# Kernel optimization log

Measured on AMD Instinct MI355X. Metric: run time of the kernel, lower is better.

Reference implementation:

```python
import jax, jax.numpy as jnp
import numpy as np

B, N, D, E, R, K = 4, 2048, 1024, 8, 256, 2


def setup_inputs() -> dict:
    key = jax.random.key(0)
    ks = jax.random.split(key, 5)
    scale = 0.02
    return {
        "x": jax.random.normal(ks[0], (B, N, D), dtype=jnp.float32),
        "gate_w": jax.random.normal(ks[1], (D, E), dtype=jnp.float32) * scale,
        "Wu": jax.random.normal(ks[2], (E, D, R), dtype=jnp.float32) * scale,
        "Wv": jax.random.normal(ks[3], (E, D, R), dtype=jnp.float32) * scale,
        "Wo": jax.random.normal(ks[4], (E, R, D), dtype=jnp.float32) * scale,
    }


def reference(x, gate_w, Wu, Wv, Wo):
    # Router: top-k over expert logits, softmax over the selected k logits.
    logits = jnp.einsum("bnd,de->bne", x, gate_w)          # [B,N,E]
    topv, topi = jax.lax.top_k(logits, K)                    # [B,N,K]
    w = jax.nn.softmax(topv, axis=-1)                        # [B,N,K]

    # Dense all-expert SwiGLU (matches reference semantics: every expert
    # computed for every token, then gathered by top-k index).
    u = jnp.einsum("bnd,edr->bner", x, Wu)                  # [B,N,E,R]
    v = jnp.einsum("bnd,edr->bner", x, Wv)                  # [B,N,E,R]
    s = jax.nn.silu(u) * v                                   # [B,N,E,R]
    Y = jnp.einsum("bner,erd->bned", s, Wo)                 # [B,N,E,D]

    # Gather the k selected experts per token and combine with gate weights.
    y_sel = jnp.take_along_axis(Y, topi[..., None], axis=2)  # [B,N,K,D]
    out = jnp.einsum("bnkd,bnk->bnd", y_sel, w)             # [B,N,D]
    return out
```

## Files before the change

kernel.cpp:

```cpp
#include <hip/hip_runtime.h>
#include <math.h>

#define BN 8192
#define DIM 1024
#define NE 8
#define RR 256

using bf16x8 = __attribute__((ext_vector_type(8))) short;
using f32x4  = __attribute__((ext_vector_type(4))) float;

__device__ inline unsigned short f2bf(float f) {
    unsigned int u = __float_as_uint(f);
    u = (u + 0x7fffu + ((u >> 16) & 1u)) >> 16;
    return (unsigned short)u;
}

__global__ __launch_bounds__(256) void k_gwt(const float* __restrict__ gw,
                                             float* __restrict__ gwT) {
    int i = blockIdx.x * 256 + threadIdx.x;
    float v = gw[i];
    int d = i >> 3, e = i & 7;
    gwT[e * DIM + d] = v;
}

__global__ __launch_bounds__(256) void k_router3(const float* __restrict__ x,
                                                 const float* __restrict__ gwT,
                                                 int* __restrict__ topi,
                                                 float* __restrict__ topw,
                                                 unsigned short* __restrict__ xb) {
    int wid  = (blockIdx.x * blockDim.x + threadIdx.x) >> 6;
    int lane = threadIdx.x & 63;
    const float* xp = x + (size_t)wid * DIM + lane * 4;
    unsigned short* xbp = xb + (size_t)wid * DIM + lane * 4;
    float4 acc[NE];
#pragma unroll
    for (int e = 0; e < NE; ++e) acc[e] = float4{0.f, 0.f, 0.f, 0.f};
#pragma unroll
    for (int k = 0; k < 4; ++k) {
        float4 xv = *(const float4*)(xp + k * 256);
        ushort4 us = { f2bf(xv.x), f2bf(xv.y), f2bf(xv.z), f2bf(xv.w) };
        *(ushort4*)(xbp + k * 256) = us;
#pragma unroll
        for (int e = 0; e < NE; ++e) {
            float4 gv = *(const float4*)(gwT + e * DIM + k * 256 + lane * 4);
            acc[e].x += xv.x * gv.x; acc[e].y += xv.y * gv.y;
            acc[e].z += xv.z * gv.z; acc[e].w += xv.w * gv.w;
        }
    }
    float lg[NE];
#pragma unroll
    for (int e = 0; e < NE; ++e)
        lg[e] = (acc[e].x + acc[e].y) + (acc[e].z + acc[e].w);
#pragma unroll
    for (int off = 32; off; off >>= 1) {
#pragma unroll
        for (int e = 0; e < NE; ++e) lg[e] += __shfl_xor(lg[e], off, 64);
    }
    if (lane == 0) {
        float best = lg[0]; int bi = 0;
#pragma unroll
        for (int e = 1; e < NE; ++e) if (lg[e] > best) { best = lg[e]; bi = e; }
        float sec = -3.4e38f; int si = 0;
#pragma unroll
        for (int e = 0; e < NE; ++e) if (e != bi && lg[e] > sec) { sec = lg[e]; si = e; }
        float p  = __expf(sec - best);
        float w0 = 1.f / (1.f + p);
        float w1 = p * w0;
        topi[wid * 2 + 0] = bi;  topw[wid * 2 + 0] = w0;
        topi[wid * 2 + 1] = si;  topw[wid * 2 + 1] = w1;
    }
}

__global__ __launch_bounds__(1024) void k_count_scan(const int* __restrict__ topi,
                                                     int* __restrict__ counts,
                                                     int* __restrict__ offsets,
                                                     int* __restrict__ fill,
                                                     int* __restrict__ tileOff) {
    __shared__ int sh[1024 * NE];
    int tid = threadIdx.x;
    int c[NE];
#pragma unroll
    for (int j = 0; j < NE; ++j) c[j] = 0;
    const int4* tp = (const int4*)topi;
    for (int i = tid; i < BN * 2 / 4; i += 1024) {
        int4 v = tp[i];
#pragma unroll
        for (int j = 0; j < NE; ++j)
            c[j] += (v.x == j) + (v.y == j) + (v.z == j) + (v.w == j);
    }
#pragma unroll
    for (int j = 0; j < NE; ++j) sh[tid * NE + j] = c[j];
    __syncthreads();
    for (int s = 512; s > 0; s >>= 1) {
        if (tid < s) {
#pragma unroll
            for (int j = 0; j < NE; ++j) sh[tid * NE + j] += sh[(tid + s) * NE + j];
        }
        __syncthreads();
    }
    if (tid == 0) {
        int acc = 0, tacc = 0;
        for (int j = 0; j < NE; ++j) {
            int cj = sh[j];
            counts[j]  = cj;
            offsets[j] = acc;   acc  += cj;
            tileOff[j] = tacc;  tacc += (cj + 63) >> 6;
        }
        tileOff[NE] = tacc;
    }
    if (tid < NE) fill[tid] = 0;
}

__global__ __launch_bounds__(256) void k_fill2(const int* __restrict__ topi,
                                               const float* __restrict__ topw,
                                               const int* __restrict__ offsets,
                                               int* __restrict__ fill,
                                               int* __restrict__ btok,
                                               float* __restrict__ bw) {
    int tid = threadIdx.x;
    int i = blockIdx.x * 256 + tid;
    int w = tid >> 6, lane = tid & 63;
    int e = topi[i];
    float wt = topw[i];

    __shared__ int waveCnt[4][NE];
    __shared__ int wavePre[4][NE];
    __shared__ int baseSh[NE];

    int myrank = 0;
    unsigned long long lt = (1ull << lane) - 1ull;
#pragma unroll
    for (int j = 0; j < NE; ++j) {
        unsigned long long m = __ballot(e == j);
        if (e == j) myrank = __popcll(m & lt);
        if (lane == 0) waveCnt[w][j] = __popcll(m);
    }
    __syncthreads();
    if (tid < NE) {
        int j = tid, acc = 0;
#pragma unroll
        for (int ww = 0; ww < 4; ++ww) { wavePre[ww][j] = acc; acc += waveCnt[ww][j]; }
        baseSh[j] = atomicAdd(&fill[j], acc);
    }
    __syncthreads();
    int slot = offsets[e] + baseSh[e] + wavePre[w][e] + myrank;
    btok[slot] = i >> 1;
    bw[slot]   = wt;
}

__global__ __launch_bounds__(256) void k_cvt3(const float* __restrict__ Wu,
                                              const float* __restrict__ Wv,
                                              const float* __restrict__ Wo,
                                              unsigned short* __restrict__ Wub,
                                              unsigned short* __restrict__ Wvb,
                                              unsigned short* __restrict__ Wob) {
    int z = blockIdx.y;
    int which = z >> 3, e = z & 7;
    int tile = blockIdx.x;
    const float* in; unsigned short* out;
    int M, N, n0, m0;
    if (which < 2) {
        M = DIM; N = RR;
        n0 = (tile & 7) * 32;  m0 = (tile >> 3) * 32;
        in = which ? Wv : Wu;  out = which ? Wvb : Wub;
    } else {
        M = RR; N = DIM;
        n0 = (tile & 31) * 32; m0 = (tile >> 5) * 32;
        in = Wo; out = Wob;
    }
    __shared__ float t[32][33];
    int tx = threadIdx.x & 31, ty = threadIdx.x >> 5;
    const float* inE = in + (size_t)e * M * N;
    unsigned short* outE = out + (size_t)e * M * N;
#pragma unroll
    for (int i = ty; i < 32; i += 8)
        t[i][tx] = inE[(size_t)(m0 + i) * N + n0 + tx];
    __syncthreads();
#pragma unroll
    for (int i = ty; i < 32; i += 8)
        outE[(size_t)(n0 + i) * M + m0 + tx] = f2bf(t[tx][i]);
}

__global__ __launch_bounds__(256, 2) void k_uv(
        const unsigned short* __restrict__ xb,
        const unsigned short* __restrict__ Wub,
        const unsigned short* __restrict__ Wvb,
        const int* __restrict__ counts,
        const int* __restrict__ offsets,
        const int* __restrict__ tileOff,
        const int* __restrict__ btok,
        const float* __restrict__ bw,
        unsigned short* __restrict__ Sbuf) {
    int rt = blockIdx.x & 3;
    int mt_lin = blockIdx.x >> 2;
    if (mt_lin >= tileOff[NE]) return;
    int e = 0;
#pragma unroll
    for (int j = 1; j < NE; ++j) if (mt_lin >= tileOff[j]) e = j;
    int t0 = (mt_lin - tileOff[e]) * 64;
    int ne = counts[e];
    int nt = min(64, ne - t0);
    int start = offsets[e] + t0;

    int tid = threadIdx.x;
    int w = tid >> 6, lane = tid & 63;
    int m16 = lane & 15, quad = lane >> 4;
    int wm = w & 1, wn = w >> 1;

    __shared__ unsigned short As[64][72];
    __shared__ unsigned short Bs[128][72];
    __shared__ int   tokL[64];
    __shared__ float gwL[64];

    if (tid < 64) {
        tokL[tid] = (tid < nt) ? btok[start + tid] : btok[start];
        gwL[tid]  = (tid < nt) ? bw[start + tid] : 0.f;
    }
    __syncthreads();

    const unsigned short* WuE = Wub + (size_t)e * RR * DIM + (size_t)rt * 64 * DIM;
    const unsigned short* WvE = Wvb + (size_t)e * RR * DIM + (size_t)rt * 64 * DIM;

    int arow = tid >> 2, apart = tid & 3;
    const unsigned short* asrc = xb + (size_t)tokL[arow] * DIM + apart * 16;
    int brow = tid >> 1, bhalf = tid & 1;
    const unsigned short* bsrc =
        (brow < 64 ? WuE + (size_t)brow * DIM : WvE + (size_t)(brow - 64) * DIM)
        + bhalf * 32;

    f32x4 accU[2][2], accV[2][2];
    f32x4 zz = {0.f, 0.f, 0.f, 0.f};
#pragma unroll
    for (int mt = 0; mt < 2; ++mt)
#pragma unroll
        for (int nl = 0; nl < 2; ++nl) { accU[mt][nl] = zz; accV[mt][nl] = zz; }

    for (int k0 = 0; k0 < DIM; k0 += 64) {
        __syncthreads();
        *(uint4*)&As[arow][apart * 16]     = *(const uint4*)(asrc + k0);
        *(uint4*)&As[arow][apart * 16 + 8] = *(const uint4*)(asrc + k0 + 8);
        *(uint4*)&Bs[brow][bhalf * 32]      = *(const uint4*)(bsrc + k0);
        *(uint4*)&Bs[brow][bhalf * 32 + 8]  = *(const uint4*)(bsrc + k0 + 8);
        *(uint4*)&Bs[brow][bhalf * 32 + 16] = *(const uint4*)(bsrc + k0 + 16);
        *(uint4*)&Bs[brow][bhalf * 32 + 24] = *(const uint4*)(bsrc + k0 + 24);
        __syncthreads();
#pragma unroll
        for (int ks = 0; ks < 2; ++ks) {
            bf16x8 a[2], bu[2], bv[2];
#pragma unroll
            for (int mt = 0; mt < 2; ++mt)
                a[mt] = *(const bf16x8*)&As[wm * 32 + mt * 16 + m16][ks * 32 + quad * 8];
#pragma unroll
            for (int nl = 0; nl < 2; ++nl) {
                bu[nl] = *(const bf16x8*)&Bs[wn * 32 + nl * 16 + m16][ks * 32 + quad * 8];
                bv[nl] = *(const bf16x8*)&Bs[64 + wn * 32 + nl * 16 + m16][ks * 32 + quad * 8];
            }
#pragma unroll
            for (int nl = 0; nl < 2; ++nl)
#pragma unroll
                for (int mt = 0; mt < 2; ++mt) {
                    accU[mt][nl] = __builtin_amdgcn_mfma_f32_16x16x32_bf16(a[mt], bu[nl], accU[mt][nl], 0, 0, 0);
                    accV[mt][nl] = __builtin_amdgcn_mfma_f32_16x16x32_bf16(a[mt], bv[nl], accV[mt][nl], 0, 0, 0);
                }
        }
    }

#pragma unroll
    for (int mt = 0; mt < 2; ++mt)
#pragma unroll
        for (int nl = 0; nl < 2; ++nl)
#pragma unroll
            for (int reg = 0; reg < 4; ++reg) {
                int trow = wm * 32 + mt * 16 + quad * 4 + reg;
                int rcol = rt * 64 + wn * 32 + nl * 16 + m16;
                float u = accU[mt][nl][reg], v = accV[mt][nl][reg];
                float s = (u / (1.f + __expf(-u))) * v * gwL[trow];
                if (trow < nt)
                    Sbuf[(size_t)(start + trow) * RR + rcol] = f2bf(s);
            }
}

__global__ __launch_bounds__(256, 2) void k_down(
        const unsigned short* __restrict__ Sbuf,
        const unsigned short* __restrict__ Wob,
        const int* __restrict__ counts,
        const int* __restrict__ offsets,
        const int* __restrict__ tileOff,
        const int* __restrict__ btok,
        float* __restrict__ out) {
    int nd = blockIdx.x & 7;
    int mt_lin = blockIdx.x >> 3;
    if (mt_lin >= tileOff[NE]) return;
    int e = 0;
#pragma unroll
    for (int j = 1; j < NE; ++j) if (mt_lin >= tileOff[j]) e = j;
    int t0 = (mt_lin - tileOff[e]) * 64;
    int ne = counts[e];
    int nt = min(64, ne - t0);
    int start = offsets[e] + t0;

    int tid = threadIdx.x;
    int w = tid >> 6, lane = tid & 63;
    int m16 = lane & 15, quad = lane >> 4;
    int wm = w & 1, wn = w >> 1;

    __shared__ unsigned short As[64][72];
    __shared__ unsigned short Bs[128][72];
    __shared__ int tokL[64];

    if (tid < 64)
        tokL[tid] = (tid < nt) ? btok[start + tid] : btok[start];
    __syncthreads();

    const unsigned short* WoE = Wob + (size_t)e * DIM * RR + (size_t)nd * 128 * RR;

    int arow = tid >> 2, apart = tid & 3;
    const unsigned short* asrc = Sbuf + (size_t)(start + arow) * RR + apart * 16;
    int brow = tid >> 1, bhalf = tid & 1;
    const unsigned short* bsrc = WoE + (size_t)brow * RR + bhalf * 32;

    f32x4 acc[2][4];
    f32x4 zz = {0.f, 0.f, 0.f, 0.f};
#pragma unroll
    for (int mt = 0; mt < 2; ++mt)
#pragma unroll
        for (int nl = 0; nl < 4; ++nl) acc[mt][nl] = zz;

    for (int k0 = 0; k0 < RR; k0 += 64) {
        __syncthreads();
        *(uint4*)&As[arow][apart * 16]     = *(const uint4*)(asrc + k0);
        *(uint4*)&As[arow][apart * 16 + 8] = *(const uint4*)(asrc + k0 + 8);
        *(uint4*)&Bs[brow][bhalf * 32]      = *(const uint4*)(bsrc + k0);
        *(uint4*)&Bs[brow][bhalf * 32 + 8]  = *(const uint4*)(bsrc + k0 + 8);
        *(uint4*)&Bs[brow][bhalf * 32 + 16] = *(const uint4*)(bsrc + k0 + 16);
        *(uint4*)&Bs[brow][bhalf * 32 + 24] = *(const uint4*)(bsrc + k0 + 24);
        __syncthreads();
#pragma unroll
        for (int ks = 0; ks < 2; ++ks) {
            bf16x8 a[2], b[4];
#pragma unroll
            for (int mt = 0; mt < 2; ++mt)
                a[mt] = *(const bf16x8*)&As[wm * 32 + mt * 16 + m16][ks * 32 + quad * 8];
#pragma unroll
            for (int nl = 0; nl < 4; ++nl)
                b[nl] = *(const bf16x8*)&Bs[wn * 64 + nl * 16 + m16][ks * 32 + quad * 8];
#pragma unroll
            for (int nl = 0; nl < 4; ++nl)
#pragma unroll
                for (int mt = 0; mt < 2; ++mt)
                    acc[mt][nl] = __builtin_amdgcn_mfma_f32_16x16x32_bf16(a[mt], b[nl], acc[mt][nl], 0, 0, 0);
        }
    }

#pragma unroll
    for (int mt = 0; mt < 2; ++mt)
#pragma unroll
        for (int nl = 0; nl < 4; ++nl)
#pragma unroll
            for (int reg = 0; reg < 4; ++reg) {
                int srow = wm * 32 + mt * 16 + quad * 4 + reg;
                int d    = nd * 128 + wn * 64 + nl * 16 + m16;
                if (srow < nt)
                    atomicAdd(&out[(size_t)tokL[srow] * DIM + d], acc[mt][nl][reg]);
            }
}

extern "C" void kernel_launch(void* const* d_in, const int* in_sizes, int n_in,
                              void* d_out, int out_size, void* d_ws, size_t ws_size,
                              hipStream_t stream) {
    const float* x  = (const float*)d_in[0];
    const float* gw = (const float*)d_in[1];
    const float* Wu = (const float*)d_in[2];
    const float* Wv = (const float*)d_in[3];
    const float* Wo = (const float*)d_in[4];
    float* out = (float*)d_out;

    int*   wsi     = (int*)d_ws;
    int*   counts  = wsi + 0;
    int*   offsets = wsi + 8;
    int*   fill    = wsi + 16;
    int*   tileOff = wsi + 24;
    int*   topi    = wsi + 48;
    float* topw    = (float*)(wsi + 48 + 16384);
    int*   btok    = wsi + 48 + 32768;
    float* bw      = (float*)(wsi + 48 + 49152);
    float* gwT     = (float*)((char*)d_ws + 327808 - 64 * 1024 + 65536);
    gwT            = (float*)((char*)d_ws + 294912);

    const size_t off_xb  = 393216;
    const size_t off_wub = off_xb  + (size_t)BN * DIM * 2;
    const size_t off_wvb = off_wub + (size_t)NE * RR * DIM * 2;
    const size_t off_wob = off_wvb + (size_t)NE * RR * DIM * 2;
    const size_t off_sb  = off_wob + (size_t)NE * DIM * RR * 2;

    unsigned short* xb   = (unsigned short*)((char*)d_ws + off_xb);
    unsigned short* Wub  = (unsigned short*)((char*)d_ws + off_wub);
    unsigned short* Wvb  = (unsigned short*)((char*)d_ws + off_wvb);
    unsigned short* Wob  = (unsigned short*)((char*)d_ws + off_wob);
    unsigned short* Sbuf = (unsigned short*)((char*)d_ws + off_sb);

    hipMemsetAsync(d_out, 0, (size_t)BN * DIM * sizeof(float), stream);

    k_gwt<<<dim3(DIM * NE / 256), 256, 0, stream>>>(gw, gwT);
    k_router3<<<dim3(BN / 4), 256, 0, stream>>>(x, gwT, topi, topw, xb);
    k_count_scan<<<1, 1024, 0, stream>>>(topi, counts, offsets, fill, tileOff);
    k_fill2<<<dim3(BN * 2 / 256), 256, 0, stream>>>(topi, topw, offsets, fill, btok, bw);
    k_cvt3<<<dim3(256, 24), 256, 0, stream>>>(Wu, Wv, Wo, Wub, Wvb, Wob);

    k_uv<<<dim3(264 * 4), 256, 0, stream>>>(xb, Wub, Wvb, counts, offsets, tileOff,
                                            btok, bw, Sbuf);
    k_down<<<dim3(264 * 8), 256, 0, stream>>>(Sbuf, Wob, counts, offsets, tileOff,
                                              btok, out);
}
```

Before: 230.4 us.

## Register-prefetch next K tile in GEMMs and replace atomic scatter with combine pass

Both grouped GEMM kernels now load the next K tile from global memory into registers while the current tile is consumed from LDS, overlapping global latency with MFMA work. The down-projection also writes per-slot results into a dense float buffer instead of atomically adding into the output. A new combine kernel then sums each token's two expert rows, which also removes the output memset. This trades atomic traffic for an extra 64 MB write and read and extra register pressure. It falls back to the atomic path when the workspace is too small.

```diff
diff --git a/kernel.cpp b/kernel.cpp
--- a/kernel.cpp
+++ b/kernel.cpp
@@ -116,7 +116,8 @@
                                                const int* __restrict__ offsets,
                                                int* __restrict__ fill,
                                                int* __restrict__ btok,
-                                               float* __restrict__ bw) {
+                                               float* __restrict__ bw,
+                                               int* __restrict__ slotOf) {
     int tid = threadIdx.x;
     int i = blockIdx.x * 256 + tid;
     int w = tid >> 6, lane = tid & 63;
@@ -146,6 +147,7 @@
     int slot = offsets[e] + baseSh[e] + wavePre[w][e] + myrank;
     btok[slot] = i >> 1;
     bw[slot]   = wt;
+    slotOf[i]  = slot;
 }
 
 __global__ __launch_bounds__(256) void k_cvt3(const float* __restrict__ Wu,
@@ -235,15 +237,31 @@
 #pragma unroll
         for (int nl = 0; nl < 2; ++nl) { accU[mt][nl] = zz; accV[mt][nl] = zz; }
 
-    for (int k0 = 0; k0 < DIM; k0 += 64) {
+    uint4 pa0 = *(const uint4*)(asrc);
+    uint4 pa1 = *(const uint4*)(asrc + 8);
+    uint4 pb0 = *(const uint4*)(bsrc);
+    uint4 pb1 = *(const uint4*)(bsrc + 8);
+    uint4 pb2 = *(const uint4*)(bsrc + 16);
+    uint4 pb3 = *(const uint4*)(bsrc + 24);
+
+    for (int kt = 0; kt < 16; ++kt) {
         __syncthreads();
-        *(uint4*)&As[arow][apart * 16]     = *(const uint4*)(asrc + k0);
-        *(uint4*)&As[arow][apart * 16 + 8] = *(const uint4*)(asrc + k0 + 8);
-        *(uint4*)&Bs[brow][bhalf * 32]      = *(const uint4*)(bsrc + k0);
-        *(uint4*)&Bs[brow][bhalf * 32 + 8]  = *(const uint4*)(bsrc + k0 + 8);
-        *(uint4*)&Bs[brow][bhalf * 32 + 16] = *(const uint4*)(bsrc + k0 + 16);
-        *(uint4*)&Bs[brow][bhalf * 32 + 24] = *(const uint4*)(bsrc + k0 + 24);
+        *(uint4*)&As[arow][apart * 16]      = pa0;
+        *(uint4*)&As[arow][apart * 16 + 8]  = pa1;
+        *(uint4*)&Bs[brow][bhalf * 32]      = pb0;
+        *(uint4*)&Bs[brow][bhalf * 32 + 8]  = pb1;
+        *(uint4*)&Bs[brow][bhalf * 32 + 16] = pb2;
+        *(uint4*)&Bs[brow][bhalf * 32 + 24] = pb3;
         __syncthreads();
+        if (kt < 15) {
+            int k1 = (kt + 1) * 64;
+            pa0 = *(const uint4*)(asrc + k1);
+            pa1 = *(const uint4*)(asrc + k1 + 8);
+            pb0 = *(const uint4*)(bsrc + k1);
+            pb1 = *(const uint4*)(bsrc + k1 + 8);
+            pb2 = *(const uint4*)(bsrc + k1 + 16);
+            pb3 = *(const uint4*)(bsrc + k1 + 24);
+        }
 #pragma unroll
         for (int ks = 0; ks < 2; ++ks) {
             bf16x8 a[2], bu[2], bv[2];
@@ -287,6 +305,7 @@
         const int* __restrict__ offsets,
         const int* __restrict__ tileOff,
         const int* __restrict__ btok,
+        float* __restrict__ ybuf,
         float* __restrict__ out) {
     int nd = blockIdx.x & 7;
     int mt_lin = blockIdx.x >> 3;
@@ -326,15 +345,31 @@
 #pragma unroll
         for (int nl = 0; nl < 4; ++nl) acc[mt][nl] = zz;
 
-    for (int k0 = 0; k0 < RR; k0 += 64) {
+    uint4 pa0 = *(const uint4*)(asrc);
+    uint4 pa1 = *(const uint4*)(asrc + 8);
+    uint4 pb0 = *(const uint4*)(bsrc);
+    uint4 pb1 = *(const uint4*)(bsrc + 8);
+    uint4 pb2 = *(const uint4*)(bsrc + 16);
+    uint4 pb3 = *(const uint4*)(bsrc + 24);
+
+    for (int kt = 0; kt < 4; ++kt) {
         __syncthreads();
-        *(uint4*)&As[arow][apart * 16]     = *(const uint4*)(asrc + k0);
-        *(uint4*)&As[arow][apart * 16 + 8] = *(const uint4*)(asrc + k0 + 8);
-        *(uint4*)&Bs[brow][bhalf * 32]      = *(const uint4*)(bsrc + k0);
-        *(uint4*)&Bs[brow][bhalf * 32 + 8]  = *(const uint4*)(bsrc + k0 + 8);
-        *(uint4*)&Bs[brow][bhalf * 32 + 16] = *(const uint4*)(bsrc + k0 + 16);
-        *(uint4*)&Bs[brow][bhalf * 32 + 24] = *(const uint4*)(bsrc + k0 + 24);
+        *(uint4*)&As[arow][apart * 16]      = pa0;
+        *(uint4*)&As[arow][apart * 16 + 8]  = pa1;
+        *(uint4*)&Bs[brow][bhalf * 32]      = pb0;
+        *(uint4*)&Bs[brow][bhalf * 32 + 8]  = pb1;
+        *(uint4*)&Bs[brow][bhalf * 32 + 16] = pb2;
+        *(uint4*)&Bs[brow][bhalf * 32 + 24] = pb3;
         __syncthreads();
+        if (kt < 3) {
+            int k1 = (kt + 1) * 64;
+            pa0 = *(const uint4*)(asrc + k1);
+            pa1 = *(const uint4*)(asrc + k1 + 8);
+            pb0 = *(const uint4*)(bsrc + k1);
+            pb1 = *(const uint4*)(bsrc + k1 + 8);
+            pb2 = *(const uint4*)(bsrc + k1 + 16);
+            pb3 = *(const uint4*)(bsrc + k1 + 24);
+        }
 #pragma unroll
         for (int ks = 0; ks < 2; ++ks) {
             bf16x8 a[2], b[4];
@@ -352,17 +387,44 @@
         }
     }
 
-#pragma unroll
-    for (int mt = 0; mt < 2; ++mt)
-#pragma unroll
-        for (int nl = 0; nl < 4; ++nl)
-#pragma unroll
-            for (int reg = 0; reg < 4; ++reg) {
-                int srow = wm * 32 + mt * 16 + quad * 4 + reg;
-                int d    = nd * 128 + wn * 64 + nl * 16 + m16;
-                if (srow < nt)
-                    atomicAdd(&out[(size_t)tokL[srow] * DIM + d], acc[mt][nl][reg]);
-            }
+    if (ybuf) {
+#pragma unroll
+        for (int mt = 0; mt < 2; ++mt)
+#pragma unroll
+            for (int nl = 0; nl < 4; ++nl)
+#pragma unroll
+                for (int reg = 0; reg < 4; ++reg) {
+                    int srow = wm * 32 + mt * 16 + quad * 4 + reg;
+                    int d    = nd * 128 + wn * 64 + nl * 16 + m16;
+                    if (srow < nt)
+                        ybuf[(size_t)(start + srow) * DIM + d] = acc[mt][nl][reg];
+                }
+    } else {
+#pragma unroll
+        for (int mt = 0; mt < 2; ++mt)
+#pragma unroll
+            for (int nl = 0; nl < 4; ++nl)
+#pragma unroll
+                for (int reg = 0; reg < 4; ++reg) {
+                    int srow = wm * 32 + mt * 16 + quad * 4 + reg;
+                    int d    = nd * 128 + wn * 64 + nl * 16 + m16;
+                    if (srow < nt)
+                        atomicAdd(&out[(size_t)tokL[srow] * DIM + d], acc[mt][nl][reg]);
+                }
+    }
+}
+
+__global__ __launch_bounds__(256) void k_combine(const float* __restrict__ ybuf,
+                                                 const int* __restrict__ slotOf,
+                                                 float* __restrict__ out) {
+    int t   = blockIdx.x;
+    int seg = threadIdx.x;
+    int s0 = slotOf[t * 2 + 0];
+    int s1 = slotOf[t * 2 + 1];
+    float4 a = *(const float4*)(ybuf + (size_t)s0 * DIM + seg * 4);
+    float4 b = *(const float4*)(ybuf + (size_t)s1 * DIM + seg * 4);
+    float4 r = { a.x + b.x, a.y + b.y, a.z + b.z, a.w + b.w };
+    *(float4*)(out + (size_t)t * DIM + seg * 4) = r;
 }
 
 extern "C" void kernel_launch(void* const* d_in, const int* in_sizes, int n_in,
@@ -384,31 +446,39 @@
     float* topw    = (float*)(wsi + 48 + 16384);
     int*   btok    = wsi + 48 + 32768;
     float* bw      = (float*)(wsi + 48 + 49152);
-    float* gwT     = (float*)((char*)d_ws + 327808 - 64 * 1024 + 65536);
-    gwT            = (float*)((char*)d_ws + 294912);
+    int*   slotOf  = wsi + 48 + 65536;
+    float* gwT     = (float*)((char*)d_ws + 327872);
 
     const size_t off_xb  = 393216;
     const size_t off_wub = off_xb  + (size_t)BN * DIM * 2;
     const size_t off_wvb = off_wub + (size_t)NE * RR * DIM * 2;
     const size_t off_wob = off_wvb + (size_t)NE * RR * DIM * 2;
     const size_t off_sb  = off_wob + (size_t)NE * DIM * RR * 2;
+    const size_t off_yb  = off_sb  + (size_t)(BN * 2 + 128) * RR * 2;
+    const size_t need_yb = off_yb  + (size_t)BN * 2 * DIM * 4;
 
     unsigned short* xb   = (unsigned short*)((char*)d_ws + off_xb);
     unsigned short* Wub  = (unsigned short*)((char*)d_ws + off_wub);
     unsigned short* Wvb  = (unsigned short*)((char*)d_ws + off_wvb);
     unsigned short* Wob  = (unsigned short*)((char*)d_ws + off_wob);
     unsigned short* Sbuf = (unsigned short*)((char*)d_ws + off_sb);
-
-    hipMemsetAsync(d_out, 0, (size_t)BN * DIM * sizeof(float), stream);
+    bool use_ybuf = (ws_size >= need_yb);
+    float* ybuf = use_ybuf ? (float*)((char*)d_ws + off_yb) : nullptr;
 
     k_gwt<<<dim3(DIM * NE / 256), 256, 0, stream>>>(gw, gwT);
     k_router3<<<dim3(BN / 4), 256, 0, stream>>>(x, gwT, topi, topw, xb);
     k_count_scan<<<1, 1024, 0, stream>>>(topi, counts, offsets, fill, tileOff);
-    k_fill2<<<dim3(BN * 2 / 256), 256, 0, stream>>>(topi, topw, offsets, fill, btok, bw);
+    k_fill2<<<dim3(BN * 2 / 256), 256, 0, stream>>>(topi, topw, offsets, fill,
+                                                    btok, bw, slotOf);
     k_cvt3<<<dim3(256, 24), 256, 0, stream>>>(Wu, Wv, Wo, Wub, Wvb, Wob);
+
+    if (!use_ybuf)
+        hipMemsetAsync(d_out, 0, (size_t)BN * DIM * sizeof(float), stream);
 
     k_uv<<<dim3(264 * 4), 256, 0, stream>>>(xb, Wub, Wvb, counts, offsets, tileOff,
                                             btok, bw, Sbuf);
     k_down<<<dim3(264 * 8), 256, 0, stream>>>(Sbuf, Wob, counts, offsets, tileOff,
-                                              btok, out);
-}
+                                              btok, ybuf, out);
+    if (use_ybuf)
+        k_combine<<<dim3(BN), 256, 0, stream>>>(ybuf, slotOf, out);
+}
```

Result: faster. 204.7 us (-11.2%).
